# Performance work log

Hardware: AMD Instinct MI355X
Metric: run time of the kernel (lower is better)

## Reference

```python
import jax, jax.numpy as jnp
import numpy as np

N = 67108864  # 64M elements, ~256 MB fp32


def setup_inputs() -> dict:
    key = jax.random.key(0)
    x = jax.random.normal(key, (N,), dtype=jnp.float32)
    return {"x": x, "bins": 256, "min": -4, "max": 4}


def reference(x, bins, min, max):
    # Faithful jnp translation of torch.histc:
    #   bin width = (max - min) / bins
    #   values in [min, max] are counted; x == max falls in the last bin;
    #   values outside the range are dropped. Output dtype matches input (float).
    lo = jnp.float32(min)
    hi = jnp.float32(max)
    width = (hi - lo) / bins
    idx = jnp.floor((x - lo) / width).astype(jnp.int32)
    # right edge is inclusive -> goes to last bin
    idx = jnp.clip(idx, 0, bins - 1)
    in_range = (x >= lo) & (x <= hi)
    w = jnp.where(in_range, jnp.float32(1.0), jnp.float32(0.0))
    hist = jnp.zeros((bins,), dtype=jnp.float32).at[idx].add(w)
    return hist
```

## Files before the change

kernel.cpp:

```cpp
#include <hip/hip_runtime.h>

#define NBINS 256
#define NWAVES 4

__global__ void zero_out_kernel(float* __restrict__ out) {
    out[threadIdx.x] = 0.0f;
}

__global__ __launch_bounds__(256) void hist_kernel(const float* __restrict__ x,
                                                   float* __restrict__ out,
                                                   int n) {
    __shared__ int lh[NWAVES][NBINS];
    const int tid  = threadIdx.x;
    const int wave = tid >> 6;

    #pragma unroll
    for (int i = tid; i < NWAVES * NBINS; i += 256)
        ((int*)lh)[i] = 0;
    __syncthreads();

    const int gid    = blockIdx.x * 256 + tid;
    const int stride = gridDim.x * 256;

    const int n4 = n >> 2;
    const float4* __restrict__ x4 = (const float4*)x;

    for (int i = gid; i < n4; i += stride) {
        float4 v = x4[i];
        float vals[4] = {v.x, v.y, v.z, v.w};
        #pragma unroll
        for (int j = 0; j < 4; ++j) {
            float f = vals[j];
            if (f >= -4.0f && f <= 4.0f) {
                int b = (int)floorf((f + 4.0f) * 32.0f);
                b = b > (NBINS - 1) ? (NBINS - 1) : b;
                atomicAdd(&lh[wave][b], 1);
            }
        }
    }

    for (int i = (n4 << 2) + gid; i < n; i += stride) {
        float f = x[i];
        if (f >= -4.0f && f <= 4.0f) {
            int b = (int)floorf((f + 4.0f) * 32.0f);
            b = b > (NBINS - 1) ? (NBINS - 1) : b;
            atomicAdd(&lh[wave][b], 1);
        }
    }

    __syncthreads();

    int s = lh[0][tid] + lh[1][tid] + lh[2][tid] + lh[3][tid];
    if (s)
        atomicAdd(&out[tid], (float)s);
}

extern "C" void kernel_launch(void* const* d_in, const int* in_sizes, int n_in,
                              void* d_out, int out_size, void* d_ws, size_t ws_size,
                              hipStream_t stream) {
    const float* x = (const float*)d_in[0];
    float* out = (float*)d_out;
    const int n = in_sizes[0];

    zero_out_kernel<<<1, NBINS, 0, stream>>>(out);

    int n4 = n >> 2;
    int blocks = (n4 + 255) / 256;
    if (blocks > 2048) blocks = 2048;
    if (blocks < 1) blocks = 1;
    hist_kernel<<<blocks, 256, 0, stream>>>(x, out, n);
}
```

Measured before the change: 89.30 us.

## Use 16 padded per-group LDS histogram copies and unroll loads by two

Replaces the four per-wave shared histograms with sixteen copies, one per 16 threads, each padded to a stride of 257 so that identical bins in different copies fall in different LDS banks. The goal is to cut same-address atomic contention and bank conflicts when many lanes hit the same bin, which is common with normally distributed input. The main loop now issues two float4 loads per iteration to raise memory-level parallelism, and floorf is replaced by a truncating cast, which is valid because the range check guarantees a non-negative value. The costs are more LDS per block and a longer zeroing and reduction phase over 16 copies.

```diff
diff --git a/kernel.cpp b/kernel.cpp
--- a/kernel.cpp
+++ b/kernel.cpp
@@ -1,7 +1,8 @@
 #include <hip/hip_runtime.h>
 
 #define NBINS 256
-#define NWAVES 4
+#define NCOPY 16
+#define CSTRIDE 257
 
 __global__ void zero_out_kernel(float* __restrict__ out) {
     out[threadIdx.x] = 0.0f;
@@ -10,47 +11,52 @@
 __global__ __launch_bounds__(256) void hist_kernel(const float* __restrict__ x,
                                                    float* __restrict__ out,
                                                    int n) {
-    __shared__ int lh[NWAVES][NBINS];
-    const int tid  = threadIdx.x;
-    const int wave = tid >> 6;
+    __shared__ int lh[NCOPY * CSTRIDE];
+    const int tid = threadIdx.x;
+    int* __restrict__ myh = &lh[(tid >> 4) * CSTRIDE];
 
-    #pragma unroll
-    for (int i = tid; i < NWAVES * NBINS; i += 256)
-        ((int*)lh)[i] = 0;
+    for (int i = tid; i < NCOPY * CSTRIDE; i += 256)
+        lh[i] = 0;
     __syncthreads();
 
     const int gid    = blockIdx.x * 256 + tid;
     const int stride = gridDim.x * 256;
-
-    const int n4 = n >> 2;
+    const int n4     = n >> 2;
     const float4* __restrict__ x4 = (const float4*)x;
 
-    for (int i = gid; i < n4; i += stride) {
-        float4 v = x4[i];
-        float vals[4] = {v.x, v.y, v.z, v.w};
-        #pragma unroll
-        for (int j = 0; j < 4; ++j) {
-            float f = vals[j];
-            if (f >= -4.0f && f <= 4.0f) {
-                int b = (int)floorf((f + 4.0f) * 32.0f);
-                b = b > (NBINS - 1) ? (NBINS - 1) : b;
-                atomicAdd(&lh[wave][b], 1);
-            }
-        }
+#define PROC(f) do {                                    \
+        float _t = ((f) + 4.0f) * 32.0f;                \
+        if ((f) >= -4.0f && (f) <= 4.0f) {              \
+            int _b = (int)_t;                           \
+            _b = _b > (NBINS - 1) ? (NBINS - 1) : _b;   \
+            atomicAdd(&myh[_b], 1);                     \
+        }                                               \
+    } while (0)
+
+    int i = gid;
+    for (; i + stride < n4; i += 2 * stride) {
+        float4 a = x4[i];
+        float4 b = x4[i + stride];
+        PROC(a.x); PROC(a.y); PROC(a.z); PROC(a.w);
+        PROC(b.x); PROC(b.y); PROC(b.z); PROC(b.w);
+    }
+    if (i < n4) {
+        float4 a = x4[i];
+        PROC(a.x); PROC(a.y); PROC(a.z); PROC(a.w);
     }
 
-    for (int i = (n4 << 2) + gid; i < n; i += stride) {
-        float f = x[i];
-        if (f >= -4.0f && f <= 4.0f) {
-            int b = (int)floorf((f + 4.0f) * 32.0f);
-            b = b > (NBINS - 1) ? (NBINS - 1) : b;
-            atomicAdd(&lh[wave][b], 1);
-        }
+    for (int j = (n4 << 2) + gid; j < n; j += stride) {
+        float f = x[j];
+        PROC(f);
     }
+#undef PROC
 
     __syncthreads();
 
-    int s = lh[0][tid] + lh[1][tid] + lh[2][tid] + lh[3][tid];
+    int s = 0;
+    #pragma unroll
+    for (int c = 0; c < NCOPY; ++c)
+        s += lh[c * CSTRIDE + tid];
     if (s)
         atomicAdd(&out[tid], (float)s);
 }
```

Measured after the change: 88.39 us. About the same (-1.0%).

## Split histogram into producer waves packing bin bytes and consumer wave doing LDS atomics

Applied to the files above, without the earlier changes.

Three waves per block load float4 data, compute bin indices, and pack four 8-bit bins per word into a double-buffered LDS ring. One consumer wave reads the ring and performs LDS atomics into four padded sub-histograms, with rejected values counted separately and subtracted from bin 0. The intent is to overlap global loads with atomic work and reduce bank conflicts via padding. The cost is that all atomics are funnelled into a single wave per block, plus a block-wide barrier every iteration.

```diff
diff --git a/kernel.cpp b/kernel.cpp
--- a/kernel.cpp
+++ b/kernel.cpp
@@ -1,56 +1,139 @@
 #include <hip/hip_runtime.h>
 
 #define NBINS 256
-#define NWAVES 4
+#define TPB 256
+#define PRODW 3
+#define PRODL (PRODW * 64)
+#define RING_W 1536
+#define GRID 2048
+
+typedef float f32x4 __attribute__((ext_vector_type(4)));
+typedef int   i32x4 __attribute__((ext_vector_type(4)));
 
 __global__ void zero_out_kernel(float* __restrict__ out) {
     out[threadIdx.x] = 0.0f;
 }
 
-__global__ __launch_bounds__(256) void hist_kernel(const float* __restrict__ x,
-                                                   float* __restrict__ out,
-                                                   int n) {
-    __shared__ int lh[NWAVES][NBINS];
+__global__ __launch_bounds__(TPB, 2) void hist_pc(const float* __restrict__ x,
+                                                  float* __restrict__ out,
+                                                  int n) {
+    __shared__ int ringw[2][RING_W];
+    __shared__ int lh[4 * 257];
+    __shared__ int rej;
     const int tid  = threadIdx.x;
     const int wave = tid >> 6;
+    const int lane = tid & 63;
 
-    #pragma unroll
-    for (int i = tid; i < NWAVES * NBINS; i += 256)
-        ((int*)lh)[i] = 0;
+    for (int i = tid; i < 4 * 257; i += TPB) lh[i] = 0;
+    if (tid == 0) rej = 0;
     __syncthreads();
 
-    const int gid    = blockIdx.x * 256 + tid;
-    const int stride = gridDim.x * 256;
+    const int n4 = n >> 2;
+    const f32x4* __restrict__ x4 = (const f32x4*)x;
+    const int PL    = gridDim.x * PRODL;
+    const int niter = n4 / (8 * PL);
 
-    const int n4 = n >> 2;
-    const float4* __restrict__ x4 = (const float4*)x;
+    if (niter > 0) {
+        if (wave > 0) {
+            const int pid  = tid - 64;
+            const int gpid = blockIdx.x * PRODL + pid;
+            int rejcnt = 0;
 
-    for (int i = gid; i < n4; i += stride) {
-        float4 v = x4[i];
-        float vals[4] = {v.x, v.y, v.z, v.w};
-        #pragma unroll
-        for (int j = 0; j < 4; ++j) {
-            float f = vals[j];
-            if (f >= -4.0f && f <= 4.0f) {
-                int b = (int)floorf((f + 4.0f) * 32.0f);
-                b = b > (NBINS - 1) ? (NBINS - 1) : b;
-                atomicAdd(&lh[wave][b], 1);
+#define BYTEOF(fv, dst) unsigned dst; {                      \
+            float _t = __builtin_fmaf((fv), 32.0f, 128.0f);  \
+            unsigned _u = (unsigned)_t;                      \
+            _u = _u > 255u ? 255u : _u;                      \
+            bool _ok = __builtin_fabsf(fv) <= 4.0f;          \
+            rejcnt += _ok ? 0 : 1;                           \
+            dst = _ok ? _u : 0u; }
+#define WORDOF(vv, res) unsigned res; {                      \
+            BYTEOF((vv).x, _b0) BYTEOF((vv).y, _b1)          \
+            BYTEOF((vv).z, _b2) BYTEOF((vv).w, _b3)          \
+            res = _b0 | (_b1 << 8) | (_b2 << 16) | (_b3 << 24); }
+
+            for (int t = 0; t < niter; ++t) {
+                const int base = t * 8 * PL + gpid;
+                f32x4 c0 = x4[base];
+                f32x4 c1 = x4[base + PL];
+                f32x4 c2 = x4[base + 2 * PL];
+                f32x4 c3 = x4[base + 3 * PL];
+                f32x4 c4 = x4[base + 4 * PL];
+                f32x4 c5 = x4[base + 5 * PL];
+                f32x4 c6 = x4[base + 6 * PL];
+                f32x4 c7 = x4[base + 7 * PL];
+                WORDOF(c0, w0) WORDOF(c1, w1) WORDOF(c2, w2) WORDOF(c3, w3)
+                WORDOF(c4, w4) WORDOF(c5, w5) WORDOF(c6, w6) WORDOF(c7, w7)
+                i32x4* dst = (i32x4*)&ringw[t & 1][pid * 8];
+                dst[0] = (i32x4){(int)w0, (int)w1, (int)w2, (int)w3};
+                dst[1] = (i32x4){(int)w4, (int)w5, (int)w6, (int)w7};
+                __syncthreads();
+            }
+#undef WORDOF
+#undef BYTEOF
+            if (rejcnt) atomicAdd(&rej, rejcnt);
+        } else {
+            int* __restrict__ myh = &lh[(lane >> 4) * 257];
+            for (int t = 0; t < niter; ++t) {
+                if (t > 0) {
+                    const int buf = (t - 1) & 1;
+                    #pragma unroll
+                    for (int r = 0; r < 6; ++r) {
+                        i32x4 v = *(const i32x4*)&ringw[buf][(r * 64 + lane) * 4];
+                        #pragma unroll
+                        for (int j = 0; j < 4; ++j) {
+                            unsigned w = (unsigned)v[j];
+                            atomicAdd(&myh[w & 255u], 1);
+                            atomicAdd(&myh[(w >> 8) & 255u], 1);
+                            atomicAdd(&myh[(w >> 16) & 255u], 1);
+                            atomicAdd(&myh[w >> 24], 1);
+                        }
+                    }
+                }
+                __syncthreads();
+            }
+            const int buf = (niter - 1) & 1;
+            #pragma unroll
+            for (int r = 0; r < 6; ++r) {
+                i32x4 v = *(const i32x4*)&ringw[buf][(r * 64 + lane) * 4];
+                #pragma unroll
+                for (int j = 0; j < 4; ++j) {
+                    unsigned w = (unsigned)v[j];
+                    atomicAdd(&myh[w & 255u], 1);
+                    atomicAdd(&myh[(w >> 8) & 255u], 1);
+                    atomicAdd(&myh[(w >> 16) & 255u], 1);
+                    atomicAdd(&myh[w >> 24], 1);
+                }
             }
         }
     }
 
-    for (int i = (n4 << 2) + gid; i < n; i += stride) {
-        float f = x[i];
-        if (f >= -4.0f && f <= 4.0f) {
-            int b = (int)floorf((f + 4.0f) * 32.0f);
-            b = b > (NBINS - 1) ? (NBINS - 1) : b;
-            atomicAdd(&lh[wave][b], 1);
+    {
+        int* __restrict__ myh2 = &lh[((tid & 63) >> 4) * 257];
+        const int gid     = blockIdx.x * TPB + tid;
+        const int gstride = gridDim.x * TPB;
+#define PROC(fv) {                                       \
+        float _t = __builtin_fmaf((fv), 32.0f, 128.0f);  \
+        unsigned _u = (unsigned)_t;                      \
+        _u = _u > 255u ? 255u : _u;                      \
+        bool _ok = __builtin_fabsf(fv) <= 4.0f;          \
+        int _b = _ok ? (int)_u : 256;                    \
+        atomicAdd(&myh2[_b], 1);                         \
+    }
+        for (int i = niter * 8 * PL + gid; i < n4; i += gstride) {
+            f32x4 a = x4[i];
+            PROC(a.x) PROC(a.y) PROC(a.z) PROC(a.w)
         }
+        for (int j = (n4 << 2) + gid; j < n; j += gstride) {
+            float f2 = x[j];
+            PROC(f2)
+        }
+#undef PROC
     }
 
     __syncthreads();
 
-    int s = lh[0][tid] + lh[1][tid] + lh[2][tid] + lh[3][tid];
+    int s = lh[tid] + lh[257 + tid] + lh[514 + tid] + lh[771 + tid];
+    if (tid == 0) s -= rej;
     if (s)
         atomicAdd(&out[tid], (float)s);
 }
@@ -64,9 +147,5 @@
 
     zero_out_kernel<<<1, NBINS, 0, stream>>>(out);
 
-    int n4 = n >> 2;
-    int blocks = (n4 + 255) / 256;
-    if (blocks > 2048) blocks = 2048;
-    if (blocks < 1) blocks = 1;
-    hist_kernel<<<blocks, 256, 0, stream>>>(x, out, n);
+    hist_pc<<<GRID, TPB, 0, stream>>>(x, out, n);
 }
```

Measured after the change: 78.81 us. 1.13x faster.
